# Kernel optimization log

Hardware: AMD Instinct MI355X
Metric: run time of the kernel (lower is better)

The kernel has to match this reference:

```python
import jax, jax.numpy as jnp
import numpy as np

N = 2048            # number_of_nodes
E = 32768           # random edges (avg degree 16); self-loops added in forward
D_IN = 3            # node attrs: uncertainty, agent_presence, target
D_PAD = 5           # padded feature width (original pads [N,3] -> [N,5] with zeros)
D_H = 3             # GAT hidden / MHA embed / TransformerConv dims
L_GAT = 10          # GAT num_layers


def _seg_softmax(logits, seg, n):
    # numerically-stable softmax over incoming edges of each destination node
    m = jax.ops.segment_max(logits, seg, num_segments=n)
    e = jnp.exp(logits - m[seg])
    s = jax.ops.segment_sum(e, seg, num_segments=n)
    return e / (s[seg] + 1e-16)


def setup_inputs() -> dict:
    key = jax.random.key(0)
    ks = jax.random.split(key, 32)
    def nrm(k, shape, scale=0.3):
        return (jax.random.normal(k, shape) * scale).astype(jnp.float32)
    return {
        "x": jax.random.uniform(ks[0], (N, D_IN), dtype=jnp.float32),
        "edge_index": jax.random.randint(ks[1], (2, E), 0, N, dtype=jnp.int32),
        "mask": jax.random.uniform(ks[2], (N,), dtype=jnp.float32),
        # 10-layer GAT (heads=1): first layer 5->3, rest 3->3
        "gat_W0": nrm(ks[3], (D_PAD, D_H)),
        "gat_W": nrm(ks[4], (L_GAT - 1, D_H, D_H)),
        "gat_att_src": nrm(ks[5], (L_GAT, D_H)),
        "gat_att_dst": nrm(ks[6], (L_GAT, D_H)),
        "gat_bias": nrm(ks[7], (L_GAT, D_H)),
        # MultiheadAttention(embed_dim=3, num_heads=3, head_dim=1)
        "mha_Wq": nrm(ks[8], (D_H, D_H)), "mha_bq": nrm(ks[9], (D_H,)),
        "mha_Wk": nrm(ks[10], (D_H, D_H)), "mha_bk": nrm(ks[11], (D_H,)),
        "mha_Wv": nrm(ks[12], (D_H, D_H)), "mha_bv": nrm(ks[13], (D_H,)),
        "mha_Wo": nrm(ks[14], (D_H, D_H)), "mha_bo": nrm(ks[15], (D_H,)),
        # TransformerConv(3 -> 3, heads=1) with root-weight skip
        "tc_Wq": nrm(ks[16], (D_H, D_H)), "tc_bq": nrm(ks[17], (D_H,)),
        "tc_Wk": nrm(ks[18], (D_H, D_H)), "tc_bk": nrm(ks[19], (D_H,)),
        "tc_Wv": nrm(ks[20], (D_H, D_H)), "tc_bv": nrm(ks[21], (D_H,)),
        "tc_Wskip": nrm(ks[22], (D_H, D_H)), "tc_bskip": nrm(ks[23], (D_H,)),
        # actor MLP (per-node; MLPAggregation with index = arange(N)): 5 -> 16 -> 32 -> 1
        "mlp_W1": nrm(ks[24], (D_PAD, 16)), "mlp_b1": nrm(ks[25], (16,)),
        "mlp_W2": nrm(ks[26], (16, 32)), "mlp_b2": nrm(ks[27], (32,)),
        "mlp_W3": nrm(ks[28], (32, 1)), "mlp_b3": nrm(ks[29], (1,)),
        # critic Linear(1, 1)
        "critic_W": nrm(ks[30], (1, 1)), "critic_b": nrm(ks[31], (1,)),
    }


def reference(x, edge_index, mask, gat_W0, gat_W, gat_att_src, gat_att_dst, gat_bias,
              mha_Wq, mha_bq, mha_Wk, mha_bk, mha_Wv, mha_bv, mha_Wo, mha_bo,
              tc_Wq, tc_bq, tc_Wk, tc_bk, tc_Wv, tc_bv, tc_Wskip, tc_bskip,
              mlp_W1, mlp_b1, mlp_W2, mlp_b2, mlp_W3, mlp_b3, critic_W, critic_b):
    n = x.shape[0]
    # pad node features [N,3] -> [N,5] with zeros, as in original forward
    h = jnp.concatenate([x, jnp.zeros((n, D_PAD - x.shape[1]), x.dtype)], axis=1)
    # add self loops (add_self_loops in original)
    loop = jnp.arange(n, dtype=edge_index.dtype)
    ei = jnp.concatenate([edge_index, jnp.stack([loop, loop])], axis=1)
    src, dst = ei[0], ei[1]
    # ---- 10-layer GAT (heads=1), ReLU between layers, none after last ----
    for l in range(L_GAT):
        W = gat_W0 if l == 0 else gat_W[l - 1]
        hW = h @ W                                   # [N, 3]
        a_s = hW @ gat_att_src[l]                    # [N]
        a_d = hW @ gat_att_dst[l]                    # [N]
        e = jax.nn.leaky_relu(a_s[src] + a_d[dst], negative_slope=0.2)
        alpha = _seg_softmax(e, dst, n)              # per-destination softmax
        h = jax.ops.segment_sum(alpha[:, None] * hW[src], dst, num_segments=n) + gat_bias[l]
        if l < L_GAT - 1:
            h = jax.nn.relu(h)
    gat_x = h                                        # [N, 3]
    # ---- self multihead attention (first call: history == [gat_x]) ----
    q = (gat_x @ mha_Wq + mha_bq).T[:, :, None]      # [H, N, 1]; head_dim = 1
    k = (gat_x @ mha_Wk + mha_bk).T[:, :, None]
    v = (gat_x @ mha_Wv + mha_bv).T[:, :, None]
    scores = jnp.einsum('hnd,hmd->hnm', q, k)        # scale = head_dim**-0.5 = 1
    attn = jax.nn.softmax(scores, axis=-1)
    ctx = jnp.einsum('hnm,hmd->hnd', attn, v)        # [H, N, 1]
    res = ctx[:, :, 0].T @ mha_Wo + mha_bo           # [N, 3]
    # ---- TransformerConv(3 -> 3, heads=1) with root skip ----
    tq = res @ tc_Wq + tc_bq
    tk = res @ tc_Wk + tc_bk
    tv = res @ tc_Wv + tc_bv
    logits = (tq[dst] * tk[src]).sum(-1) / jnp.sqrt(3.0)
    alpha = _seg_softmax(logits, dst, n)
    agg = jax.ops.segment_sum(alpha[:, None] * tv[src], dst, num_segments=n)
    out = agg + res @ tc_Wskip + tc_bskip            # [N, 3]
    # pad again to 5 channels
    out5 = jnp.concatenate([out, jnp.zeros((n, D_PAD - out.shape[1]), out.dtype)], axis=1)
    # ---- actor: per-node MLP (MLPAggregation, index = arange(N) -> identity batching) ----
    h1 = jax.nn.relu(out5 @ mlp_W1 + mlp_b1)
    h2 = jax.nn.relu(h1 @ mlp_W2 + mlp_b2)
    results = h2 @ mlp_W3 + mlp_b3                   # [N, 1]
    new_results = results[:, 0] * mask               # [N]
    value = (results @ critic_W + critic_b).mean()   # scalar
    return new_results, value
```

## Files before the change

kernel.cpp:

```cpp
#include <hip/hip_runtime.h>
#include <cstdint>

#define NN   2048
#define EIN  32768
#define NB   64
#define BT   1024
#define OPB  32
#define ECAP 2048
#define UCAP 1024
#define EPT  (EIN / BT)
#define RS3  0.5773502691896258f
#define SENT 0xFFFFFFFFu

#define WS_TICKET 0
#define WS_H      128
#define WS_TKA    (WS_H + 10*NN*16)
#define WS_TKB    (WS_TKA + NN*16)
#define WS_VPART  (WS_TKB + NN*8)
#define WS_END    (WS_VPART + 256)

static __device__ __forceinline__ uint64_t cload64(const void* p) {
    return __hip_atomic_load((const uint64_t*)p, __ATOMIC_RELAXED, __HIP_MEMORY_SCOPE_AGENT);
}
static __device__ __forceinline__ void cstore64(void* p, uint64_t v) {
    __hip_atomic_store((uint64_t*)p, v, __ATOMIC_RELAXED, __HIP_MEMORY_SCOPE_AGENT);
}
static __device__ __forceinline__ void cstoref4(float4* p, float4 v) {
    union { float4 f; uint64_t u[2]; } c; c.f = v;
    cstore64(p, c.u[0]); cstore64((char*)p + 8, c.u[1]);
}
static __device__ __forceinline__ void cstoref2(float2* p, float2 v) {
    union { float2 f; uint64_t u; } c; c.f = v; cstore64(p, c.u);
}
static __device__ __forceinline__ void cstoref(float* p, float v) {
    union { float f; uint32_t u; } c; c.f = v;
    __hip_atomic_store((uint32_t*)p, c.u, __ATOMIC_RELAXED, __HIP_MEMORY_SCOPE_AGENT);
}
static __device__ __forceinline__ float4 pollf4(const float4* p) {
    uint64_t a = cload64(p);
    uint64_t b = cload64((const char*)p + 8);
    while ((uint32_t)a == SENT || (uint32_t)b == SENT) {
        __builtin_amdgcn_s_sleep(1);
        a = cload64(p);
        b = cload64((const char*)p + 8);
    }
    union { uint64_t u[2]; float4 f; } c; c.u[0] = a; c.u[1] = b;
    return c.f;
}
static __device__ __forceinline__ float2 pollf2(const float2* p) {
    uint64_t a = cload64(p);
    while ((uint32_t)a == SENT) { __builtin_amdgcn_s_sleep(1); a = cload64(p); }
    union { uint64_t u; float2 f; } c; c.u = a;
    return c.f;
}
static __device__ __forceinline__ float pollf(const float* p) {
    uint32_t a = __hip_atomic_load((const uint32_t*)p, __ATOMIC_RELAXED, __HIP_MEMORY_SCOPE_AGENT);
    while (a == SENT) {
        __builtin_amdgcn_s_sleep(1);
        a = __hip_atomic_load((const uint32_t*)p, __ATOMIC_RELAXED, __HIP_MEMORY_SCOPE_AGENT);
    }
    union { uint32_t u; float f; } c; c.u = a;
    return c.f;
}

__global__ __launch_bounds__(BT) void k_fused(
    const float* __restrict__ x, const int* __restrict__ ei,
    const float* __restrict__ maskp,
    const float* __restrict__ gW0, const float* __restrict__ gW,
    const float* __restrict__ atts, const float* __restrict__ attd,
    const float* __restrict__ gbias,
    const float* __restrict__ mWq, const float* __restrict__ mbq,
    const float* __restrict__ mWk, const float* __restrict__ mbk,
    const float* __restrict__ mWv, const float* __restrict__ mbv,
    const float* __restrict__ mWo, const float* __restrict__ mbo,
    const float* __restrict__ tWq, const float* __restrict__ tbq,
    const float* __restrict__ tWk, const float* __restrict__ tbk,
    const float* __restrict__ tWv, const float* __restrict__ tbv,
    const float* __restrict__ tWs, const float* __restrict__ tbs,
    const float* __restrict__ W1, const float* __restrict__ b1,
    const float* __restrict__ W2, const float* __restrict__ b2,
    const float* __restrict__ W3, const float* __restrict__ b3,
    const float* __restrict__ cW, const float* __restrict__ cb,
    char* __restrict__ ws, float* __restrict__ outp)
{
    __shared__ __align__(16) char pool[49152];
    __shared__ float4 hw4L[UCAP];
    __shared__ unsigned short srcs[ECAP];
    __shared__ unsigned short uniq[UCAP];
    __shared__ unsigned short mark[NN];
    __shared__ int offs[OPB + 1];
    __shared__ int cntL[OPB], curL[OPB], dloc[OPB];
    __shared__ int uniqCnt;
    __shared__ float4 ownH[OPB], tqL[OPB], skipL[OPB];
    __shared__ float ctxL[3][OPB];
    __shared__ float redf[96];
    __shared__ float resL[OPB];
    __shared__ float Mhd[6];

    int*    ticket = (int*)(ws + WS_TICKET);
    float4* hbase  = (float4*)(ws + WS_H);
    float4* tka    = (float4*)(ws + WS_TKA);
    float2* tkb    = (float2*)(ws + WS_TKB);
    float*  vpart  = (float*)(ws + WS_VPART);

    const int tid  = threadIdx.x;
    const int bid  = blockIdx.x;
    const int lane = tid & 63;
    const int wid  = tid >> 6;
    const int R0   = bid * OPB;

    int dcache[EPT];
    #pragma unroll
    for (int i = 0; i < EPT; ++i) dcache[i] = ei[EIN + tid + i * BT];

    if (tid < OPB) cntL[tid] = 1;
    __syncthreads();
    #pragma unroll
    for (int i = 0; i < EPT; ++i) {
        unsigned rel = (unsigned)(dcache[i] - R0);
        if (rel < OPB) atomicAdd(&cntL[rel], 1);
    }
    __syncthreads();
    if (tid < 64) {
        int c = (tid < OPB) ? cntL[tid] : 0;
        int v = c;
        #pragma unroll
        for (int d = 1; d < 32; d <<= 1) {
            int u = __shfl_up(v, d);
            if (tid >= d) v += u;
        }
        if (tid < OPB) {
            offs[tid + 1] = v;
            curL[tid] = v - c + 1;
            srcs[v - c] = (unsigned short)(R0 + tid);
        }
        if (tid == 0) { offs[0] = 0; uniqCnt = 0; }
    }
    __syncthreads();
    #pragma unroll
    for (int i = 0; i < EPT; ++i) {
        unsigned rel = (unsigned)(dcache[i] - R0);
        if (rel < OPB) {
            int p = atomicAdd(&curL[rel], 1);
            srcs[p] = (unsigned short)ei[tid + i * BT];
        }
    }
    mark[tid] = 0xFFFFu; mark[tid + BT] = 0xFFFFu;
    __syncthreads();

    const int totE = offs[OPB];
    for (int p = tid; p < totE; p += BT) {
        int s = srcs[p];
        if (mark[s] == 0xFFFFu) {
            int u = atomicAdd(&uniqCnt, 1);
            uniq[u] = (unsigned short)s;
            mark[s] = (unsigned short)u;
        }
    }
    __syncthreads();
    for (int p = tid; p < totE; p += BT) srcs[p] = mark[srcs[p]];
    if (tid < OPB) dloc[tid] = mark[R0 + tid];
    __syncthreads();
    const int UC = uniqCnt;

    for (int l = 0; l < 10; ++l) {
        const float4* hprev = hbase + (l - 1) * NN;
        float4*       hnext = hbase + l * NN;
        const float* W = l ? (gW + (l - 1) * 9) : gW0;
        float w00=W[0],w01=W[1],w02=W[2],w10=W[3],w11=W[4],w12=W[5],w20=W[6],w21=W[7],w22=W[8];
        float s0=atts[3*l],s1=atts[3*l+1],s2=atts[3*l+2];
        float d0=attd[3*l],d1=attd[3*l+1],d2=attd[3*l+2];
        float bb0=gbias[3*l],bb1=gbias[3*l+1],bb2=gbias[3*l+2];
        if (tid < UC) {
            int g = uniq[tid];
            float hx, hy, hz;
            if (l == 0) { hx = x[3*g]; hy = x[3*g+1]; hz = x[3*g+2]; }
            else { float4 t = pollf4(&hprev[g]); hx = t.x; hy = t.y; hz = t.z; }
            float p0 = fmaf(hx, w00, fmaf(hy, w10, hz * w20));
            float p1 = fmaf(hx, w01, fmaf(hy, w11, hz * w21));
            float p2 = fmaf(hx, w02, fmaf(hy, w12, hz * w22));
            hw4L[tid] = make_float4(p0, p1, p2, fmaf(p0, s0, fmaf(p1, s1, p2 * s2)));
        }
        __syncthreads();
        {
            int j = tid >> 5, sub = tid & 31;
            int ps = offs[j], pe = offs[j + 1];
            float4 hd = hw4L[dloc[j]];
            float ad = fmaf(hd.x, d0, fmaf(hd.y, d1, hd.z * d2));
            float m = -1e30f;
            for (int p = ps + sub; p < pe; p += 32) {
                float lg = hw4L[srcs[p]].w + ad;
                lg = (lg > 0.f) ? lg : 0.2f * lg;
                m = fmaxf(m, lg);
            }
            #pragma unroll
            for (int d = 1; d < 32; d <<= 1) m = fmaxf(m, __shfl_xor(m, d));
            float se = 0.f, a0 = 0.f, a1 = 0.f, a2 = 0.f;
            for (int p = ps + sub; p < pe; p += 32) {
                float4 hs = hw4L[srcs[p]];
                float lg = hs.w + ad;
                lg = (lg > 0.f) ? lg : 0.2f * lg;
                float e = __expf(lg - m);
                se += e;
                a0 = fmaf(e, hs.x, a0);
                a1 = fmaf(e, hs.y, a1);
                a2 = fmaf(e, hs.z, a2);
            }
            #pragma unroll
            for (int d = 1; d < 32; d <<= 1) {
                se += __shfl_xor(se, d);
                a0 += __shfl_xor(a0, d);
                a1 += __shfl_xor(a1, d);
                a2 += __shfl_xor(a2, d);
            }
            if (sub == 0) {
                float inv = 1.f / (se + 1e-16f);
                float o0 = a0*inv + bb0;
                float o1 = a1*inv + bb1;
                float o2 = a2*inv + bb2;
                if (l < 9) { o0 = fmaxf(o0,0.f); o1 = fmaxf(o1,0.f); o2 = fmaxf(o2,0.f); }
                cstoref4(&hnext[R0 + j], make_float4(o0, o1, o2, 0.f));
            }
        }
        __syncthreads();
    }

    {
        const float4* hf = hbase + 9 * NN;
        float* kk = (float*)pool;
        float* vv = (float*)(pool + 24576);
        float kmx[3] = {-3e38f,-3e38f,-3e38f}, kmn[3] = {3e38f,3e38f,3e38f};
        #pragma unroll
        for (int i = 0; i < 2; ++i) {
            int n = tid + i * BT;
            float4 g = pollf4(&hf[n]);
            unsigned rel = (unsigned)(n - R0);
            if (rel < OPB) ownH[rel] = g;
            #pragma unroll
            for (int c = 0; c < 3; ++c) {
                float kv = fmaf(g.x, mWk[c], fmaf(g.y, mWk[3+c], fmaf(g.z, mWk[6+c], mbk[c])));
                float vvv= fmaf(g.x, mWv[c], fmaf(g.y, mWv[3+c], fmaf(g.z, mWv[6+c], mbv[c])));
                kk[c*NN + n] = kv; vv[c*NN + n] = vvv;
                kmx[c] = fmaxf(kmx[c], kv); kmn[c] = fminf(kmn[c], kv);
            }
        }
        #pragma unroll
        for (int c = 0; c < 3; ++c) {
            #pragma unroll
            for (int d = 1; d < 64; d <<= 1) {
                kmx[c] = fmaxf(kmx[c], __shfl_xor(kmx[c], d));
                kmn[c] = fminf(kmn[c], __shfl_xor(kmn[c], d));
            }
        }
        if (lane == 0) {
            #pragma unroll
            for (int c = 0; c < 3; ++c) {
                redf[wid*6 + c]     = kmx[c];
                redf[wid*6 + 3 + c] = kmn[c];
            }
        }
        __syncthreads();
        if (tid < 6) {
            bool ismax = tid < 3;
            float acc = ismax ? -3e38f : 3e38f;
            for (int w2 = 0; w2 < 16; ++w2) {
                float t = redf[w2*6 + tid];
                acc = ismax ? fmaxf(acc, t) : fminf(acc, t);
            }
            Mhd[tid] = acc;
        }
        __syncthreads();
        #pragma unroll
        for (int jr = 0; jr < 6; ++jr) {
            int r = wid * 6 + jr;
            int h = r >> 5, i2 = r & 31;
            float4 g = ownH[i2];
            float q = fmaf(g.x, mWq[h], fmaf(g.y, mWq[3+h], fmaf(g.z, mWq[6+h], mbq[h])));
            float M = (q >= 0.f) ? q * Mhd[h] : q * Mhd[3 + h];
            const float* kp = kk + h * NN;
            const float* vp = vv + h * NN;
            float sse = 0.f, ssv = 0.f;
            for (int mc = lane; mc < NN; mc += 64) {
                float e = __expf(fmaf(q, kp[mc], -M));
                sse += e; ssv = fmaf(e, vp[mc], ssv);
            }
            #pragma unroll
            for (int d = 32; d; d >>= 1) {
                sse += __shfl_xor(sse, d); ssv += __shfl_xor(ssv, d);
            }
            if (lane == 0) ctxL[h][i2] = ssv / sse;
        }
        __syncthreads();
        if (tid < OPB) {
            int n = R0 + tid;
            float c0 = ctxL[0][tid], c1 = ctxL[1][tid], c2 = ctxL[2][tid];
            float r0 = fmaf(c0, mWo[0], fmaf(c1, mWo[3], fmaf(c2, mWo[6], mbo[0])));
            float r1 = fmaf(c0, mWo[1], fmaf(c1, mWo[4], fmaf(c2, mWo[7], mbo[1])));
            float r2 = fmaf(c0, mWo[2], fmaf(c1, mWo[5], fmaf(c2, mWo[8], mbo[2])));
            float q0 = fmaf(r0, tWq[0], fmaf(r1, tWq[3], fmaf(r2, tWq[6], tbq[0])));
            float q1 = fmaf(r0, tWq[1], fmaf(r1, tWq[4], fmaf(r2, tWq[7], tbq[1])));
            float q2 = fmaf(r0, tWq[2], fmaf(r1, tWq[5], fmaf(r2, tWq[8], tbq[2])));
            tqL[tid] = make_float4(q0, q1, q2, 0.f);
            float k0 = fmaf(r0, tWk[0], fmaf(r1, tWk[3], fmaf(r2, tWk[6], tbk[0])));
            float k1 = fmaf(r0, tWk[1], fmaf(r1, tWk[4], fmaf(r2, tWk[7], tbk[1])));
            float k2 = fmaf(r0, tWk[2], fmaf(r1, tWk[5], fmaf(r2, tWk[8], tbk[2])));
            float v0 = fmaf(r0, tWv[0], fmaf(r1, tWv[3], fmaf(r2, tWv[6], tbv[0])));
            float v1 = fmaf(r0, tWv[1], fmaf(r1, tWv[4], fmaf(r2, tWv[7], tbv[1])));
            float v2 = fmaf(r0, tWv[2], fmaf(r1, tWv[5], fmaf(r2, tWv[8], tbv[2])));
            cstoref4(&tka[n], make_float4(k0, k1, k2, v0));
            cstoref2(&tkb[n], make_float2(v1, v2));
            float s0 = fmaf(r0, tWs[0], fmaf(r1, tWs[3], fmaf(r2, tWs[6], tbs[0])));
            float s1 = fmaf(r0, tWs[1], fmaf(r1, tWs[4], fmaf(r2, tWs[7], tbs[1])));
            float s2 = fmaf(r0, tWs[2], fmaf(r1, tWs[5], fmaf(r2, tWs[8], tbs[2])));
            skipL[tid] = make_float4(s0, s1, s2, 0.f);
        }
    }

    {
        float4* sAL = (float4*)pool;
        float2* sBL = (float2*)(pool + 16384);
        if (tid < UC) {
            int g = uniq[tid];
            sAL[tid] = pollf4(&tka[g]);
            sBL[tid] = pollf2(&tkb[g]);
        }
        __syncthreads();
        int j = tid >> 5, sub = tid & 31;
        float4 qv = tqL[j];
        int ps = offs[j], pe = offs[j + 1];
        float m = -1e30f;
        for (int p = ps + sub; p < pe; p += 32) {
            float4 A = sAL[srcs[p]];
            float lg = fmaf(qv.x, A.x, fmaf(qv.y, A.y, qv.z * A.z)) * RS3;
            m = fmaxf(m, lg);
        }
        #pragma unroll
        for (int d = 1; d < 32; d <<= 1) m = fmaxf(m, __shfl_xor(m, d));
        float se = 0.f, a0 = 0.f, a1 = 0.f, a2 = 0.f;
        for (int p = ps + sub; p < pe; p += 32) {
            int s = srcs[p];
            float4 A = sAL[s];
            float2 B = sBL[s];
            float lg = fmaf(qv.x, A.x, fmaf(qv.y, A.y, qv.z * A.z)) * RS3;
            float e = __expf(lg - m);
            se += e;
            a0 = fmaf(e, A.w, a0);
            a1 = fmaf(e, B.x, a1);
            a2 = fmaf(e, B.y, a2);
        }
        #pragma unroll
        for (int d = 1; d < 32; d <<= 1) {
            se += __shfl_xor(se, d);
            a0 += __shfl_xor(a0, d);
            a1 += __shfl_xor(a1, d);
            a2 += __shfl_xor(a2, d);
        }
        float inv = 1.f / (se + 1e-16f);
        float4 sk = skipL[j];
        float o0 = a0*inv + sk.x;
        float o1 = a1*inv + sk.y;
        float o2 = a2*inv + sk.z;
        float h1v[16];
        #pragma unroll
        for (int k = 0; k < 16; ++k)
            h1v[k] = fmaxf(fmaf(o0, W1[k], fmaf(o1, W1[16+k], fmaf(o2, W1[32+k], b1[k]))), 0.f);
        float t = b2[sub];
        #pragma unroll
        for (int k = 0; k < 16; ++k) t = fmaf(h1v[k], W2[k*32 + sub], t);
        float racc = fmaxf(t, 0.f) * W3[sub];
        #pragma unroll
        for (int d = 1; d < 32; d <<= 1) racc += __shfl_xor(racc, d);
        float resv = racc + b3[0];
        if (sub == 0) {
            int n = R0 + j;
            outp[n] = resv * maskp[n];
            resL[j] = resv;
        }
        __syncthreads();
        if (tid == 0) {
            float s = 0.f;
            for (int u = 0; u < OPB; ++u) s += resL[u];
            cstoref(&vpart[bid], s);
            int tk = __hip_atomic_fetch_add(ticket, 1, __ATOMIC_RELAXED, __HIP_MEMORY_SCOPE_AGENT);
            if (tk == NB - 1) {
                float tsum = 0.f;
                for (int b = 0; b < NB; ++b) tsum += pollf(&vpart[b]);
                outp[NN] = fmaf(cW[0], tsum * (1.f / (float)NN), cb[0]);
            }
        }
    }
}

extern "C" void kernel_launch(void* const* d_in, const int* in_sizes, int n_in,
                              void* d_out, int out_size, void* d_ws, size_t ws_size,
                              hipStream_t stream)
{
    const float* x    = (const float*)d_in[0];
    const int*   ei   = (const int*)  d_in[1];
    const float* mask = (const float*)d_in[2];
    const float* gW0  = (const float*)d_in[3];
    const float* gW   = (const float*)d_in[4];
    const float* atts = (const float*)d_in[5];
    const float* attd = (const float*)d_in[6];
    const float* gbias= (const float*)d_in[7];
    const float* mWq = (const float*)d_in[8];  const float* mbq = (const float*)d_in[9];
    const float* mWk = (const float*)d_in[10]; const float* mbk = (const float*)d_in[11];
    const float* mWv = (const float*)d_in[12]; const float* mbv = (const float*)d_in[13];
    const float* mWo = (const float*)d_in[14]; const float* mbo = (const float*)d_in[15];
    const float* tWq = (const float*)d_in[16]; const float* tbq = (const float*)d_in[17];
    const float* tWk = (const float*)d_in[18]; const float* tbk = (const float*)d_in[19];
    const float* tWv = (const float*)d_in[20]; const float* tbv = (const float*)d_in[21];
    const float* tWs = (const float*)d_in[22]; const float* tbs = (const float*)d_in[23];
    const float* W1  = (const float*)d_in[24]; const float* b1  = (const float*)d_in[25];
    const float* W2  = (const float*)d_in[26]; const float* b2  = (const float*)d_in[27];
    const float* W3  = (const float*)d_in[28]; const float* b3  = (const float*)d_in[29];
    const float* cW  = (const float*)d_in[30]; const float* cb  = (const float*)d_in[31];

    hipMemsetAsync(d_ws, 0, 128, stream);
    hipMemsetAsync((char*)d_ws + WS_H, 0xFF, WS_END - WS_H, stream);

    k_fused<<<NB, BT, 0, stream>>>(x, ei, mask, gW0, gW, atts, attd, gbias,
                                   mWq, mbq, mWk, mbk, mWv, mbv, mWo, mbo,
                                   tWq, tbq, tWk, tbk, tWv, tbv, tWs, tbs,
                                   W1, b1, W2, b2, W3, b3, cW, cb,
                                   (char*)d_ws, (float*)d_out);
}
```

Before: 80.86 us.

## Pair GAT layers per block using 2-hop neighborhoods and global barriers

Each block now builds the two-hop in-neighborhood of its 32 owned nodes and computes two GAT layers locally: all unique neighbors for the first layer of a pair, then its own nodes for the second. Only every other layer is published to global memory, which halves the number of cross-block synchronisation points. Per-element sentinel polling is replaced by flag-based grid barriers, and the workspace memset shrinks to the flag and ticket region. In exchange each block does redundant neighbor-layer work, and the second-hop edge list is capped at a fixed size, so edges beyond that cap would be silently dropped.

```diff
diff --git a/kernel.cpp b/kernel.cpp
--- a/kernel.cpp
+++ b/kernel.cpp
@@ -1,66 +1,67 @@
 #include <hip/hip_runtime.h>
 #include <cstdint>
 
-#define NN   2048
-#define EIN  32768
-#define NB   64
-#define BT   1024
-#define OPB  32
-#define ECAP 2048
-#define UCAP 1024
-#define EPT  (EIN / BT)
-#define RS3  0.5773502691896258f
-#define SENT 0xFFFFFFFFu
-
-#define WS_TICKET 0
-#define WS_H      128
-#define WS_TKA    (WS_H + 10*NN*16)
+#define NN    2048
+#define EIN   32768
+#define NB    64
+#define BT    1024
+#define OPB   32
+#define EPT   (EIN / BT)
+#define ECAP  2048
+#define UCAP  1024
+#define E2CAP 10240
+#define RS3   0.5773502691896258f
+
+#define WS_FLAGS  0
+#define WS_TICKET 8192
+#define WS_HPUB   8448
+#define WS_TKA    (WS_HPUB + 5*NN*16)
 #define WS_TKB    (WS_TKA + NN*16)
 #define WS_VPART  (WS_TKB + NN*8)
-#define WS_END    (WS_VPART + 256)
 
 static __device__ __forceinline__ uint64_t cload64(const void* p) {
     return __hip_atomic_load((const uint64_t*)p, __ATOMIC_RELAXED, __HIP_MEMORY_SCOPE_AGENT);
 }
 static __device__ __forceinline__ void cstore64(void* p, uint64_t v) {
     __hip_atomic_store((uint64_t*)p, v, __ATOMIC_RELAXED, __HIP_MEMORY_SCOPE_AGENT);
+}
+static __device__ __forceinline__ float4 cloadf4(const float4* p) {
+    union { float4 f; uint64_t u[2]; } c;
+    c.u[0] = cload64(p); c.u[1] = cload64((const char*)p + 8);
+    return c.f;
 }
 static __device__ __forceinline__ void cstoref4(float4* p, float4 v) {
     union { float4 f; uint64_t u[2]; } c; c.f = v;
     cstore64(p, c.u[0]); cstore64((char*)p + 8, c.u[1]);
 }
+static __device__ __forceinline__ float2 cloadf2(const float2* p) {
+    union { float2 f; uint64_t u; } c; c.u = cload64(p); return c.f;
+}
 static __device__ __forceinline__ void cstoref2(float2* p, float2 v) {
     union { float2 f; uint64_t u; } c; c.f = v; cstore64(p, c.u);
+}
+static __device__ __forceinline__ float cloadf(const float* p) {
+    union { float f; uint32_t u; } c;
+    c.u = __hip_atomic_load((const uint32_t*)p, __ATOMIC_RELAXED, __HIP_MEMORY_SCOPE_AGENT);
+    return c.f;
 }
 static __device__ __forceinline__ void cstoref(float* p, float v) {
     union { float f; uint32_t u; } c; c.f = v;
     __hip_atomic_store((uint32_t*)p, c.u, __ATOMIC_RELAXED, __HIP_MEMORY_SCOPE_AGENT);
 }
-static __device__ __forceinline__ float4 pollf4(const float4* p) {
-    uint64_t a = cload64(p);
-    uint64_t b = cload64((const char*)p + 8);
-    while ((uint32_t)a == SENT || (uint32_t)b == SENT) {
-        __builtin_amdgcn_s_sleep(1);
-        a = cload64(p);
-        b = cload64((const char*)p + 8);
-    }
-    union { uint64_t u[2]; float4 f; } c; c.u[0] = a; c.u[1] = b;
-    return c.f;
-}
-static __device__ __forceinline__ float2 pollf2(const float2* p) {
-    uint64_t a = cload64(p);
-    while ((uint32_t)a == SENT) { __builtin_amdgcn_s_sleep(1); a = cload64(p); }
-    union { uint64_t u; float2 f; } c; c.u = a;
-    return c.f;
-}
-static __device__ __forceinline__ float pollf(const float* p) {
-    uint32_t a = __hip_atomic_load((const uint32_t*)p, __ATOMIC_RELAXED, __HIP_MEMORY_SCOPE_AGENT);
-    while (a == SENT) {
-        __builtin_amdgcn_s_sleep(1);
-        a = __hip_atomic_load((const uint32_t*)p, __ATOMIC_RELAXED, __HIP_MEMORY_SCOPE_AGENT);
-    }
-    union { uint32_t u; float f; } c; c.u = a;
-    return c.f;
+
+static __device__ __forceinline__ void gbar(int* flags, int bid, int phase) {
+    __syncthreads();
+    if (threadIdx.x < 64) {
+        if (threadIdx.x == 0) {
+            asm volatile("s_waitcnt vmcnt(0)" ::: "memory");
+            __hip_atomic_store(&flags[bid * 32], phase, __ATOMIC_RELAXED, __HIP_MEMORY_SCOPE_AGENT);
+        }
+        while (__hip_atomic_load(&flags[threadIdx.x * 32], __ATOMIC_RELAXED,
+                                 __HIP_MEMORY_SCOPE_AGENT) < phase)
+            __builtin_amdgcn_s_sleep(1);
+    }
+    __syncthreads();
 }
 
 __global__ __launch_bounds__(BT) void k_fused(
@@ -83,25 +84,33 @@
     const float* __restrict__ cW, const float* __restrict__ cb,
     char* __restrict__ ws, float* __restrict__ outp)
 {
-    __shared__ __align__(16) char pool[49152];
-    __shared__ float4 hw4L[UCAP];
+    __shared__ __align__(16) char uni[53248];
+    __shared__ float4 hI[UCAP];
+    __shared__ int    offs2[UCAP + 1];
+    __shared__ int    cnt2[UCAP];
+    __shared__ unsigned short mark[NN];
+    __shared__ unsigned short uniq[UCAP];
     __shared__ unsigned short srcs[ECAP];
-    __shared__ unsigned short uniq[UCAP];
-    __shared__ unsigned short mark[NN];
-    __shared__ int offs[OPB + 1];
-    __shared__ int cntL[OPB], curL[OPB], dloc[OPB];
-    __shared__ int uniqCnt;
+    __shared__ int   offs[OPB + 1];
+    __shared__ int   cntL[OPB];
+    __shared__ int   dloc[OPB];
+    __shared__ int   uniqCnt;
+    __shared__ int   redi[16];
+    __shared__ float redf[96];
     __shared__ float4 ownH[OPB], tqL[OPB], skipL[OPB];
     __shared__ float ctxL[3][OPB];
-    __shared__ float redf[96];
     __shared__ float resL[OPB];
     __shared__ float Mhd[6];
 
-    int*    ticket = (int*)(ws + WS_TICKET);
-    float4* hbase  = (float4*)(ws + WS_H);
-    float4* tka    = (float4*)(ws + WS_TKA);
-    float2* tkb    = (float2*)(ws + WS_TKB);
-    float*  vpart  = (float*)(ws + WS_VPART);
+    int*    flags = (int*)(ws + WS_FLAGS);
+    int*    ticket= (int*)(ws + WS_TICKET);
+    float4* hpub  = (float4*)(ws + WS_HPUB);
+    float4* tka   = (float4*)(ws + WS_TKA);
+    float2* tkb   = (float2*)(ws + WS_TKB);
+    float*  vpart = (float*)(ws + WS_VPART);
+
+    float4* hw4F = (float4*)uni;
+    unsigned short* srcs2 = (unsigned short*)(uni + 32768);
 
     const int tid  = threadIdx.x;
     const int bid  = blockIdx.x;
@@ -131,7 +140,7 @@
         }
         if (tid < OPB) {
             offs[tid + 1] = v;
-            curL[tid] = v - c + 1;
+            cntL[tid] = v - c + 1;
             srcs[v - c] = (unsigned short)(R0 + tid);
         }
         if (tid == 0) { offs[0] = 0; uniqCnt = 0; }
@@ -141,7 +150,7 @@
     for (int i = 0; i < EPT; ++i) {
         unsigned rel = (unsigned)(dcache[i] - R0);
         if (rel < OPB) {
-            int p = atomicAdd(&curL[rel], 1);
+            int p = atomicAdd(&cntL[rel], 1);
             srcs[p] = (unsigned short)ei[tid + i * BT];
         }
     }
@@ -163,33 +172,139 @@
     __syncthreads();
     const int UC = uniqCnt;
 
-    for (int l = 0; l < 10; ++l) {
-        const float4* hprev = hbase + (l - 1) * NN;
-        float4*       hnext = hbase + l * NN;
-        const float* W = l ? (gW + (l - 1) * 9) : gW0;
-        float w00=W[0],w01=W[1],w02=W[2],w10=W[3],w11=W[4],w12=W[5],w20=W[6],w21=W[7],w22=W[8];
-        float s0=atts[3*l],s1=atts[3*l+1],s2=atts[3*l+2];
-        float d0=attd[3*l],d1=attd[3*l+1],d2=attd[3*l+2];
-        float bb0=gbias[3*l],bb1=gbias[3*l+1],bb2=gbias[3*l+2];
+    cnt2[tid] = (tid < UC) ? 1 : 0;
+    __syncthreads();
+    #pragma unroll
+    for (int i = 0; i < EPT; ++i) {
+        int ld = mark[dcache[i]];
+        if (ld != 0xFFFF) atomicAdd(&cnt2[ld], 1);
+    }
+    __syncthreads();
+    {
+        int c = cnt2[tid];
+        int v = c;
+        #pragma unroll
+        for (int d = 1; d < 64; d <<= 1) {
+            int u = __shfl_up(v, d);
+            if (lane >= d) v += u;
+        }
+        if (lane == 63) redi[wid] = v;
+        __syncthreads();
+        if (wid == 0 && lane < 16) {
+            int t = redi[lane];
+            #pragma unroll
+            for (int d = 1; d < 16; d <<= 1) {
+                int u = __shfl_up(t, d);
+                if (lane >= d) t += u;
+            }
+            redi[lane] = t;
+        }
+        __syncthreads();
+        int base = (wid ? redi[wid - 1] : 0) + (v - c);
+        offs2[tid + 1] = base + c;
+        if (tid == 0) offs2[0] = 0;
         if (tid < UC) {
-            int g = uniq[tid];
-            float hx, hy, hz;
-            if (l == 0) { hx = x[3*g]; hy = x[3*g+1]; hz = x[3*g+2]; }
-            else { float4 t = pollf4(&hprev[g]); hx = t.x; hy = t.y; hz = t.z; }
-            float p0 = fmaf(hx, w00, fmaf(hy, w10, hz * w20));
-            float p1 = fmaf(hx, w01, fmaf(hy, w11, hz * w21));
-            float p2 = fmaf(hx, w02, fmaf(hy, w12, hz * w22));
-            hw4L[tid] = make_float4(p0, p1, p2, fmaf(p0, s0, fmaf(p1, s1, p2 * s2)));
-        }
-        __syncthreads();
+            cnt2[tid] = base + 1;
+            srcs2[base] = uniq[tid];
+        }
+    }
+    __syncthreads();
+    #pragma unroll
+    for (int i = 0; i < EPT; ++i) {
+        int ld = mark[dcache[i]];
+        if (ld != 0xFFFF) {
+            int p = atomicAdd(&cnt2[ld], 1);
+            if (p < E2CAP) srcs2[p] = (unsigned short)ei[tid + i * BT];
+        }
+    }
+    __syncthreads();
+
+    for (int g = 0; g < 5; ++g) {
+        const int l0 = 2 * g, l1 = l0 + 1;
         {
+            const float* W = l0 ? (gW + (l0 - 1) * 9) : gW0;
+            float w00=W[0],w01=W[1],w02=W[2],w10=W[3],w11=W[4],w12=W[5],w20=W[6],w21=W[7],w22=W[8];
+            float s0=atts[3*l0],s1=atts[3*l0+1],s2=atts[3*l0+2];
+            const float4* hin = hpub + (g - 1) * NN;
+            #pragma unroll
+            for (int i = 0; i < 2; ++i) {
+                int n = tid + i * BT;
+                float hx, hy, hz;
+                if (g == 0) { hx = x[3*n]; hy = x[3*n+1]; hz = x[3*n+2]; }
+                else { float4 t = cloadf4(&hin[n]); hx = t.x; hy = t.y; hz = t.z; }
+                float p0 = fmaf(hx, w00, fmaf(hy, w10, hz * w20));
+                float p1 = fmaf(hx, w01, fmaf(hy, w11, hz * w21));
+                float p2 = fmaf(hx, w02, fmaf(hy, w12, hz * w22));
+                hw4F[n] = make_float4(p0, p1, p2, fmaf(p0, s0, fmaf(p1, s1, p2 * s2)));
+            }
+        }
+        __syncthreads();
+        {
+            float d0=attd[3*l0],d1=attd[3*l0+1],d2=attd[3*l0+2];
+            float bb0=gbias[3*l0],bb1=gbias[3*l0+1],bb2=gbias[3*l0+2];
+            int grp = tid >> 4, sub = tid & 15;
+            for (int jd = grp; jd < UC; jd += 64) {
+                int ps = offs2[jd], pe = offs2[jd + 1];
+                float4 hd = hw4F[uniq[jd]];
+                float ad = fmaf(hd.x, d0, fmaf(hd.y, d1, hd.z * d2));
+                float m = -1e30f;
+                for (int p = ps + sub; p < pe; p += 16) {
+                    float lg = hw4F[srcs2[p]].w + ad;
+                    lg = (lg > 0.f) ? lg : 0.2f * lg;
+                    m = fmaxf(m, lg);
+                }
+                #pragma unroll
+                for (int d = 1; d < 16; d <<= 1) m = fmaxf(m, __shfl_xor(m, d));
+                float se = 0.f, a0 = 0.f, a1 = 0.f, a2 = 0.f;
+                for (int p = ps + sub; p < pe; p += 16) {
+                    float4 hs = hw4F[srcs2[p]];
+                    float lg = hs.w + ad;
+                    lg = (lg > 0.f) ? lg : 0.2f * lg;
+                    float e = __expf(lg - m);
+                    se += e;
+                    a0 = fmaf(e, hs.x, a0);
+                    a1 = fmaf(e, hs.y, a1);
+                    a2 = fmaf(e, hs.z, a2);
+                }
+                #pragma unroll
+                for (int d = 1; d < 16; d <<= 1) {
+                    se += __shfl_xor(se, d);
+                    a0 += __shfl_xor(a0, d);
+                    a1 += __shfl_xor(a1, d);
+                    a2 += __shfl_xor(a2, d);
+                }
+                if (sub == 0) {
+                    float inv = 1.f / (se + 1e-16f);
+                    hI[jd] = make_float4(fmaxf(a0*inv + bb0, 0.f),
+                                         fmaxf(a1*inv + bb1, 0.f),
+                                         fmaxf(a2*inv + bb2, 0.f), 0.f);
+                }
+            }
+        }
+        __syncthreads();
+        {
+            const float* W = gW + (l1 - 1) * 9;
+            float w00=W[0],w01=W[1],w02=W[2],w10=W[3],w11=W[4],w12=W[5],w20=W[6],w21=W[7],w22=W[8];
+            float s0=atts[3*l1],s1=atts[3*l1+1],s2=atts[3*l1+2];
+            if (tid < UC) {
+                float4 t = hI[tid];
+                float p0 = fmaf(t.x, w00, fmaf(t.y, w10, t.z * w20));
+                float p1 = fmaf(t.x, w01, fmaf(t.y, w11, t.z * w21));
+                float p2 = fmaf(t.x, w02, fmaf(t.y, w12, t.z * w22));
+                hw4F[tid] = make_float4(p0, p1, p2, fmaf(p0, s0, fmaf(p1, s1, p2 * s2)));
+            }
+        }
+        __syncthreads();
+        {
+            float d0=attd[3*l1],d1=attd[3*l1+1],d2=attd[3*l1+2];
+            float bb0=gbias[3*l1],bb1=gbias[3*l1+1],bb2=gbias[3*l1+2];
             int j = tid >> 5, sub = tid & 31;
             int ps = offs[j], pe = offs[j + 1];
-            float4 hd = hw4L[dloc[j]];
+            float4 hd = hw4F[dloc[j]];
             float ad = fmaf(hd.x, d0, fmaf(hd.y, d1, hd.z * d2));
             float m = -1e30f;
             for (int p = ps + sub; p < pe; p += 32) {
-                float lg = hw4L[srcs[p]].w + ad;
+                float lg = hw4F[srcs[p]].w + ad;
                 lg = (lg > 0.f) ? lg : 0.2f * lg;
                 m = fmaxf(m, lg);
             }
@@ -197,7 +312,7 @@
             for (int d = 1; d < 32; d <<= 1) m = fmaxf(m, __shfl_xor(m, d));
             float se = 0.f, a0 = 0.f, a1 = 0.f, a2 = 0.f;
             for (int p = ps + sub; p < pe; p += 32) {
-                float4 hs = hw4L[srcs[p]];
+                float4 hs = hw4F[srcs[p]];
                 float lg = hs.w + ad;
                 lg = (lg > 0.f) ? lg : 0.2f * lg;
                 float e = __expf(lg - m);
@@ -218,29 +333,28 @@
                 float o0 = a0*inv + bb0;
                 float o1 = a1*inv + bb1;
                 float o2 = a2*inv + bb2;
-                if (l < 9) { o0 = fmaxf(o0,0.f); o1 = fmaxf(o1,0.f); o2 = fmaxf(o2,0.f); }
-                cstoref4(&hnext[R0 + j], make_float4(o0, o1, o2, 0.f));
-            }
-        }
-        __syncthreads();
+                if (l1 < 9) { o0 = fmaxf(o0,0.f); o1 = fmaxf(o1,0.f); o2 = fmaxf(o2,0.f); }
+                cstoref4(&hpub[g * NN + R0 + j], make_float4(o0, o1, o2, 0.f));
+            }
+        }
+        gbar(flags, bid, g + 1);
     }
 
     {
-        const float4* hf = hbase + 9 * NN;
-        float* kk = (float*)pool;
-        float* vv = (float*)(pool + 24576);
+        const float4* h9 = hpub + 4 * NN;
+        float2* kvh = (float2*)uni;
         float kmx[3] = {-3e38f,-3e38f,-3e38f}, kmn[3] = {3e38f,3e38f,3e38f};
         #pragma unroll
         for (int i = 0; i < 2; ++i) {
             int n = tid + i * BT;
-            float4 g = pollf4(&hf[n]);
+            float4 g4 = cloadf4(&h9[n]);
             unsigned rel = (unsigned)(n - R0);
-            if (rel < OPB) ownH[rel] = g;
+            if (rel < OPB) ownH[rel] = g4;
             #pragma unroll
             for (int c = 0; c < 3; ++c) {
-                float kv = fmaf(g.x, mWk[c], fmaf(g.y, mWk[3+c], fmaf(g.z, mWk[6+c], mbk[c])));
-                float vvv= fmaf(g.x, mWv[c], fmaf(g.y, mWv[3+c], fmaf(g.z, mWv[6+c], mbv[c])));
-                kk[c*NN + n] = kv; vv[c*NN + n] = vvv;
+                float kv = fmaf(g4.x, mWk[c], fmaf(g4.y, mWk[3+c], fmaf(g4.z, mWk[6+c], mbk[c])));
+                float vv = fmaf(g4.x, mWv[c], fmaf(g4.y, mWv[3+c], fmaf(g4.z, mWv[6+c], mbv[c])));
+                kvh[c*NN + n] = make_float2(kv, vv);
                 kmx[c] = fmaxf(kmx[c], kv); kmn[c] = fminf(kmn[c], kv);
             }
         }
@@ -274,15 +388,15 @@
         for (int jr = 0; jr < 6; ++jr) {
             int r = wid * 6 + jr;
             int h = r >> 5, i2 = r & 31;
-            float4 g = ownH[i2];
-            float q = fmaf(g.x, mWq[h], fmaf(g.y, mWq[3+h], fmaf(g.z, mWq[6+h], mbq[h])));
+            float4 g4 = ownH[i2];
+            float q = fmaf(g4.x, mWq[h], fmaf(g4.y, mWq[3+h], fmaf(g4.z, mWq[6+h], mbq[h])));
             float M = (q >= 0.f) ? q * Mhd[h] : q * Mhd[3 + h];
-            const float* kp = kk + h * NN;
-            const float* vp = vv + h * NN;
+            const float2* kp = kvh + h * NN;
             float sse = 0.f, ssv = 0.f;
             for (int mc = lane; mc < NN; mc += 64) {
-                float e = __expf(fmaf(q, kp[mc], -M));
-                sse += e; ssv = fmaf(e, vp[mc], ssv);
+                float2 kv = kp[mc];
+                float e = __expf(fmaf(q, kv.x, -M));
+                sse += e; ssv = fmaf(e, kv.y, ssv);
             }
             #pragma unroll
             for (int d = 32; d; d >>= 1) {
@@ -315,14 +429,15 @@
             skipL[tid] = make_float4(s0, s1, s2, 0.f);
         }
     }
+    gbar(flags, bid, 6);
 
     {
-        float4* sAL = (float4*)pool;
-        float2* sBL = (float2*)(pool + 16384);
+        float4* sAL = (float4*)uni;
+        float2* sBL = (float2*)(uni + 16384);
         if (tid < UC) {
             int g = uniq[tid];
-            sAL[tid] = pollf4(&tka[g]);
-            sBL[tid] = pollf2(&tkb[g]);
+            sAL[tid] = cloadf4(&tka[g]);
+            sBL[tid] = cloadf2(&tkb[g]);
         }
         __syncthreads();
         int j = tid >> 5, sub = tid & 31;
@@ -381,10 +496,11 @@
             float s = 0.f;
             for (int u = 0; u < OPB; ++u) s += resL[u];
             cstoref(&vpart[bid], s);
+            asm volatile("s_waitcnt vmcnt(0)" ::: "memory");
             int tk = __hip_atomic_fetch_add(ticket, 1, __ATOMIC_RELAXED, __HIP_MEMORY_SCOPE_AGENT);
             if (tk == NB - 1) {
                 float tsum = 0.f;
-                for (int b = 0; b < NB; ++b) tsum += pollf(&vpart[b]);
+                for (int b = 0; b < NB; ++b) tsum += cloadf(&vpart[b]);
                 outp[NN] = fmaf(cW[0], tsum * (1.f / (float)NN), cb[0]);
             }
         }
@@ -416,8 +532,7 @@
     const float* W3  = (const float*)d_in[28]; const float* b3  = (const float*)d_in[29];
     const float* cW  = (const float*)d_in[30]; const float* cb  = (const float*)d_in[31];
 
-    hipMemsetAsync(d_ws, 0, 128, stream);
-    hipMemsetAsync((char*)d_ws + WS_H, 0xFF, WS_END - WS_H, stream);
+    hipMemsetAsync(d_ws, 0, 8448, stream);
 
     k_fused<<<NB, BT, 0, stream>>>(x, ei, mask, gW0, gW, atts, attd, gbias,
                                    mWq, mbq, mWk, mbk, mWv, mbv, mWo, mbo,
```

Measured after the change: 134.2 us. +65.9%, slower.

## Replace per-element sentinel polling with flag-based grid barriers and ping-pong buffers

Applied to the files above, without the earlier changes.

Swaps the per-node sentinel polling (which needed a large 0xFF memset of all layer buffers) for an explicit grid barrier built from per-block phase flags after each GAT layer and before the TransformerConv stage. Layer outputs now alternate between two buffers instead of ten, which shrinks the workspace memset to the flag and ticket region. It also interleaves the MHA K and V values into float2 pairs in shared memory and re-reads edge destinations from global memory instead of caching them in registers. The cost is that every block now waits for the slowest block at each layer, where before it only waited on the rows it needed, and correctness depends on all 64 blocks being co-resident.

```diff
diff --git a/kernel.cpp b/kernel.cpp
--- a/kernel.cpp
+++ b/kernel.cpp
@@ -8,59 +8,61 @@
 #define OPB  32
 #define ECAP 2048
 #define UCAP 1024
-#define EPT  (EIN / BT)
 #define RS3  0.5773502691896258f
-#define SENT 0xFFFFFFFFu
-
-#define WS_TICKET 0
-#define WS_H      128
-#define WS_TKA    (WS_H + 10*NN*16)
-#define WS_TKB    (WS_TKA + NN*16)
-#define WS_VPART  (WS_TKB + NN*8)
-#define WS_END    (WS_VPART + 256)
+
+#define WS_FLAGS 0
+#define WS_TICKET 8192
+#define WS_HA    8448
+#define WS_HB    41216
+#define WS_TKA   73984
+#define WS_TKB   106752
+#define WS_VPART 123136
+#define WS_MEMSET_BYTES 8196
 
 static __device__ __forceinline__ uint64_t cload64(const void* p) {
     return __hip_atomic_load((const uint64_t*)p, __ATOMIC_RELAXED, __HIP_MEMORY_SCOPE_AGENT);
 }
 static __device__ __forceinline__ void cstore64(void* p, uint64_t v) {
     __hip_atomic_store((uint64_t*)p, v, __ATOMIC_RELAXED, __HIP_MEMORY_SCOPE_AGENT);
+}
+static __device__ __forceinline__ float4 cloadf4(const float4* p) {
+    union { float4 f; uint64_t u[2]; } c;
+    c.u[0] = cload64(p); c.u[1] = cload64((const char*)p + 8);
+    return c.f;
 }
 static __device__ __forceinline__ void cstoref4(float4* p, float4 v) {
     union { float4 f; uint64_t u[2]; } c; c.f = v;
     cstore64(p, c.u[0]); cstore64((char*)p + 8, c.u[1]);
 }
+static __device__ __forceinline__ float2 cloadf2(const float2* p) {
+    union { float2 f; uint64_t u; } c; c.u = cload64(p); return c.f;
+}
 static __device__ __forceinline__ void cstoref2(float2* p, float2 v) {
     union { float2 f; uint64_t u; } c; c.f = v; cstore64(p, c.u);
+}
+static __device__ __forceinline__ float cloadf(const float* p) {
+    union { float f; uint32_t u; } c;
+    c.u = __hip_atomic_load((const uint32_t*)p, __ATOMIC_RELAXED, __HIP_MEMORY_SCOPE_AGENT);
+    return c.f;
 }
 static __device__ __forceinline__ void cstoref(float* p, float v) {
     union { float f; uint32_t u; } c; c.f = v;
     __hip_atomic_store((uint32_t*)p, c.u, __ATOMIC_RELAXED, __HIP_MEMORY_SCOPE_AGENT);
 }
-static __device__ __forceinline__ float4 pollf4(const float4* p) {
-    uint64_t a = cload64(p);
-    uint64_t b = cload64((const char*)p + 8);
-    while ((uint32_t)a == SENT || (uint32_t)b == SENT) {
-        __builtin_amdgcn_s_sleep(1);
-        a = cload64(p);
-        b = cload64((const char*)p + 8);
-    }
-    union { uint64_t u[2]; float4 f; } c; c.u[0] = a; c.u[1] = b;
-    return c.f;
-}
-static __device__ __forceinline__ float2 pollf2(const float2* p) {
-    uint64_t a = cload64(p);
-    while ((uint32_t)a == SENT) { __builtin_amdgcn_s_sleep(1); a = cload64(p); }
-    union { uint64_t u; float2 f; } c; c.u = a;
-    return c.f;
-}
-static __device__ __forceinline__ float pollf(const float* p) {
-    uint32_t a = __hip_atomic_load((const uint32_t*)p, __ATOMIC_RELAXED, __HIP_MEMORY_SCOPE_AGENT);
-    while (a == SENT) {
-        __builtin_amdgcn_s_sleep(1);
-        a = __hip_atomic_load((const uint32_t*)p, __ATOMIC_RELAXED, __HIP_MEMORY_SCOPE_AGENT);
-    }
-    union { uint32_t u; float f; } c; c.u = a;
-    return c.f;
+
+static __device__ __forceinline__ void gbar(int* flags, int bid, int phase) {
+    __syncthreads();
+    if (threadIdx.x < 64) {
+        if (threadIdx.x == 0) {
+            asm volatile("s_waitcnt vmcnt(0)" ::: "memory");
+            __hip_atomic_exchange(&flags[bid * 32], phase, __ATOMIC_RELAXED,
+                                  __HIP_MEMORY_SCOPE_AGENT);
+        }
+        while (__hip_atomic_load(&flags[threadIdx.x * 32], __ATOMIC_RELAXED,
+                                 __HIP_MEMORY_SCOPE_AGENT) < phase)
+            __builtin_amdgcn_s_sleep(1);
+    }
+    __syncthreads();
 }
 
 __global__ __launch_bounds__(BT) void k_fused(
@@ -97,8 +99,10 @@
     __shared__ float resL[OPB];
     __shared__ float Mhd[6];
 
+    int*    flags  = (int*)(ws + WS_FLAGS);
     int*    ticket = (int*)(ws + WS_TICKET);
-    float4* hbase  = (float4*)(ws + WS_H);
+    float4* ha     = (float4*)(ws + WS_HA);
+    float4* hb     = (float4*)(ws + WS_HB);
     float4* tka    = (float4*)(ws + WS_TKA);
     float2* tkb    = (float2*)(ws + WS_TKB);
     float*  vpart  = (float*)(ws + WS_VPART);
@@ -109,15 +113,10 @@
     const int wid  = tid >> 6;
     const int R0   = bid * OPB;
 
-    int dcache[EPT];
-    #pragma unroll
-    for (int i = 0; i < EPT; ++i) dcache[i] = ei[EIN + tid + i * BT];
-
     if (tid < OPB) cntL[tid] = 1;
     __syncthreads();
-    #pragma unroll
-    for (int i = 0; i < EPT; ++i) {
-        unsigned rel = (unsigned)(dcache[i] - R0);
+    for (int e = tid; e < EIN; e += BT) {
+        unsigned rel = (unsigned)(ei[EIN + e] - R0);
         if (rel < OPB) atomicAdd(&cntL[rel], 1);
     }
     __syncthreads();
@@ -137,12 +136,11 @@
         if (tid == 0) { offs[0] = 0; uniqCnt = 0; }
     }
     __syncthreads();
-    #pragma unroll
-    for (int i = 0; i < EPT; ++i) {
-        unsigned rel = (unsigned)(dcache[i] - R0);
+    for (int e = tid; e < EIN; e += BT) {
+        unsigned rel = (unsigned)(ei[EIN + e] - R0);
         if (rel < OPB) {
             int p = atomicAdd(&curL[rel], 1);
-            srcs[p] = (unsigned short)ei[tid + i * BT];
+            srcs[p] = (unsigned short)ei[e];
         }
     }
     mark[tid] = 0xFFFFu; mark[tid + BT] = 0xFFFFu;
@@ -164,8 +162,8 @@
     const int UC = uniqCnt;
 
     for (int l = 0; l < 10; ++l) {
-        const float4* hprev = hbase + (l - 1) * NN;
-        float4*       hnext = hbase + l * NN;
+        float4* hprev = (l & 1) ? ha : hb;
+        float4* hcur  = (l & 1) ? hb : ha;
         const float* W = l ? (gW + (l - 1) * 9) : gW0;
         float w00=W[0],w01=W[1],w02=W[2],w10=W[3],w11=W[4],w12=W[5],w20=W[6],w21=W[7],w22=W[8];
         float s0=atts[3*l],s1=atts[3*l+1],s2=atts[3*l+2];
@@ -175,7 +173,7 @@
             int g = uniq[tid];
             float hx, hy, hz;
             if (l == 0) { hx = x[3*g]; hy = x[3*g+1]; hz = x[3*g+2]; }
-            else { float4 t = pollf4(&hprev[g]); hx = t.x; hy = t.y; hz = t.z; }
+            else { float4 t = cloadf4(&hprev[g]); hx = t.x; hy = t.y; hz = t.z; }
             float p0 = fmaf(hx, w00, fmaf(hy, w10, hz * w20));
             float p1 = fmaf(hx, w01, fmaf(hy, w11, hz * w21));
             float p2 = fmaf(hx, w02, fmaf(hy, w12, hz * w22));
@@ -219,28 +217,26 @@
                 float o1 = a1*inv + bb1;
                 float o2 = a2*inv + bb2;
                 if (l < 9) { o0 = fmaxf(o0,0.f); o1 = fmaxf(o1,0.f); o2 = fmaxf(o2,0.f); }
-                cstoref4(&hnext[R0 + j], make_float4(o0, o1, o2, 0.f));
-            }
-        }
-        __syncthreads();
+                cstoref4(&hcur[R0 + j], make_float4(o0, o1, o2, 0.f));
+            }
+        }
+        gbar(flags, bid, l + 1);
     }
 
     {
-        const float4* hf = hbase + 9 * NN;
-        float* kk = (float*)pool;
-        float* vv = (float*)(pool + 24576);
+        float2* kvh = (float2*)pool;
         float kmx[3] = {-3e38f,-3e38f,-3e38f}, kmn[3] = {3e38f,3e38f,3e38f};
         #pragma unroll
         for (int i = 0; i < 2; ++i) {
             int n = tid + i * BT;
-            float4 g = pollf4(&hf[n]);
+            float4 g = cloadf4(&hb[n]);
             unsigned rel = (unsigned)(n - R0);
             if (rel < OPB) ownH[rel] = g;
             #pragma unroll
             for (int c = 0; c < 3; ++c) {
                 float kv = fmaf(g.x, mWk[c], fmaf(g.y, mWk[3+c], fmaf(g.z, mWk[6+c], mbk[c])));
-                float vvv= fmaf(g.x, mWv[c], fmaf(g.y, mWv[3+c], fmaf(g.z, mWv[6+c], mbv[c])));
-                kk[c*NN + n] = kv; vv[c*NN + n] = vvv;
+                float vv = fmaf(g.x, mWv[c], fmaf(g.y, mWv[3+c], fmaf(g.z, mWv[6+c], mbv[c])));
+                kvh[c*NN + n] = make_float2(kv, vv);
                 kmx[c] = fmaxf(kmx[c], kv); kmn[c] = fminf(kmn[c], kv);
             }
         }
@@ -277,12 +273,12 @@
             float4 g = ownH[i2];
             float q = fmaf(g.x, mWq[h], fmaf(g.y, mWq[3+h], fmaf(g.z, mWq[6+h], mbq[h])));
             float M = (q >= 0.f) ? q * Mhd[h] : q * Mhd[3 + h];
-            const float* kp = kk + h * NN;
-            const float* vp = vv + h * NN;
+            const float2* kp = kvh + h * NN;
             float sse = 0.f, ssv = 0.f;
             for (int mc = lane; mc < NN; mc += 64) {
-                float e = __expf(fmaf(q, kp[mc], -M));
-                sse += e; ssv = fmaf(e, vp[mc], ssv);
+                float2 kv = kp[mc];
+                float e = __expf(fmaf(q, kv.x, -M));
+                sse += e; ssv = fmaf(e, kv.y, ssv);
             }
             #pragma unroll
             for (int d = 32; d; d >>= 1) {
@@ -315,14 +311,15 @@
             skipL[tid] = make_float4(s0, s1, s2, 0.f);
         }
     }
+    gbar(flags, bid, 11);
 
     {
         float4* sAL = (float4*)pool;
         float2* sBL = (float2*)(pool + 16384);
         if (tid < UC) {
             int g = uniq[tid];
-            sAL[tid] = pollf4(&tka[g]);
-            sBL[tid] = pollf2(&tkb[g]);
+            sAL[tid] = cloadf4(&tka[g]);
+            sBL[tid] = cloadf2(&tkb[g]);
         }
         __syncthreads();
         int j = tid >> 5, sub = tid & 31;
@@ -381,10 +378,11 @@
             float s = 0.f;
             for (int u = 0; u < OPB; ++u) s += resL[u];
             cstoref(&vpart[bid], s);
+            asm volatile("s_waitcnt vmcnt(0)" ::: "memory");
             int tk = __hip_atomic_fetch_add(ticket, 1, __ATOMIC_RELAXED, __HIP_MEMORY_SCOPE_AGENT);
             if (tk == NB - 1) {
                 float tsum = 0.f;
-                for (int b = 0; b < NB; ++b) tsum += pollf(&vpart[b]);
+                for (int b = 0; b < NB; ++b) tsum += cloadf(&vpart[b]);
                 outp[NN] = fmaf(cW[0], tsum * (1.f / (float)NN), cb[0]);
             }
         }
@@ -416,8 +414,7 @@
     const float* W3  = (const float*)d_in[28]; const float* b3  = (const float*)d_in[29];
     const float* cW  = (const float*)d_in[30]; const float* cb  = (const float*)d_in[31];
 
-    hipMemsetAsync(d_ws, 0, 128, stream);
-    hipMemsetAsync((char*)d_ws + WS_H, 0xFF, WS_END - WS_H, stream);
+    hipMemsetAsync(d_ws, 0, WS_MEMSET_BYTES, stream);
 
     k_fused<<<NB, BT, 0, stream>>>(x, ei, mask, gW0, gW, atts, attd, gbias,
                                    mWq, mbq, mWk, mbk, mWv, mbv, mWo, mbo,
```

Result: slower. 84.80 us (+4.9%).
